# Performance work log

Hardware: AMD Instinct MI355X
Metric: run time of the kernel (lower is better)

## Reference

```python
import jax, jax.numpy as jnp
import numpy as np

B, S = 4096, 8192

def setup_inputs() -> dict:
    key = jax.random.key(0)
    c = jax.random.normal(key, (B, S), dtype=jnp.float32)
    beta = jnp.asarray(10.0, dtype=jnp.float32)
    return {"c": c, "beta": beta}

def reference(c, beta):
    # Original per-step recurrence:
    #   delta_i = (1/beta) * logsumexp([beta*delta_{i-1}, beta*(c_i + delta_{i-1})])
    #           = delta_{i-1} + (1/beta) * log(1 + exp(beta * c_i))
    # i.e. an exact prefix sum of softplus(beta*c)/beta along S.
    # (Note: the torch code stacks delta_prev, not 0, as the first branch,
    #  so the logsumexp telescopes to a cumulative sum.)
    step = jax.nn.softplus(beta * c) / beta          # (B, S)
    return jnp.cumsum(step, axis=1)                  # (B, S) propagated delays
```

## Files before the change

### kernel.cpp

```cpp
#include <hip/hip_runtime.h>
#include <hip/hip_bf16.h>


#define ROW_S   8192
#define BLOCK_T 256
#define NJ      (ROW_S / 4 / BLOCK_T)
#define NWAVE   (BLOCK_T / 64)

__device__ __forceinline__ float softplus_step(float c, float beta, float inv_beta) {
    float tb = beta * c;
    float a  = fabsf(tb);
    float e  = __expf(-a);
    float l  = __logf(1.0f + e);
    return (fmaxf(tb, 0.0f) + l) * inv_beta;
}

__global__ __launch_bounds__(BLOCK_T) void softplus_cumsum_kernel(
    const float* __restrict__ c,
    const float* __restrict__ beta_p,
    float* __restrict__ out)
{
    __shared__ float wave_sums[NJ][NWAVE];

    const int t    = threadIdx.x;
    const int lane = t & 63;
    const int wave = t >> 6;
    const size_t row_base = (size_t)blockIdx.x * ROW_S;

    const float beta     = beta_p[0];
    const float inv_beta = 1.0f / beta;

    const float4* __restrict__ in4  = (const float4*)(c + row_base);
    float4*       __restrict__ out4 = (float4*)(out + row_base);

    float4 v[NJ];
    #pragma unroll
    for (int j = 0; j < NJ; ++j)
        v[j] = in4[j * BLOCK_T + t];

    float4 r[NJ];
    float  s[NJ];
    #pragma unroll
    for (int j = 0; j < NJ; ++j) {
        float a = softplus_step(v[j].x, beta, inv_beta);
        float b = softplus_step(v[j].y, beta, inv_beta);
        float d = softplus_step(v[j].z, beta, inv_beta);
        float e = softplus_step(v[j].w, beta, inv_beta);
        r[j].x = a;
        r[j].y = a + b;
        r[j].z = r[j].y + d;
        r[j].w = r[j].z + e;
        s[j]   = r[j].w;
    }

    float xscan[NJ];
    #pragma unroll
    for (int j = 0; j < NJ; ++j) {
        float x = s[j];
        #pragma unroll
        for (int d = 1; d < 64; d <<= 1) {
            float y = __shfl_up(x, d, 64);
            if (lane >= d) x += y;
        }
        xscan[j] = x;
        if (lane == 63) wave_sums[j][wave] = x;
    }
    __syncthreads();

    float carry = 0.0f;
    #pragma unroll
    for (int j = 0; j < NJ; ++j) {
        float woff = 0.0f, btot = 0.0f;
        #pragma unroll
        for (int w = 0; w < NWAVE; ++w) {
            float ws = wave_sums[j][w];
            if (w < wave) woff += ws;
            btot += ws;
        }
        const float off = carry + woff + (xscan[j] - s[j]);
        carry += btot;

        float4 o;
        o.x = r[j].x + off;
        o.y = r[j].y + off;
        o.z = r[j].z + off;
        o.w = r[j].w + off;
        out4[j * BLOCK_T + t] = o;
    }
}

extern "C" void kernel_launch(void* const* d_in, const int* in_sizes, int n_in,
                              void* d_out, int out_size, void* d_ws, size_t ws_size,
                              hipStream_t stream) {
    const float* c      = (const float*)d_in[0];
    const float* beta_p = (const float*)d_in[1];
    float*       out    = (float*)d_out;

    const int B = in_sizes[0] / ROW_S;
    softplus_cumsum_kernel<<<dim3(B), dim3(BLOCK_T), 0, stream>>>(c, beta_p, out);
}
```

Before: 233.1 us.

## Process four rows per block with register double-buffered prefetch of next row

Each block now handles RPB=4 rows strided by gridDim, issuing the loads for the next row before computing the scan on the current one so memory latency overlaps compute. Wave sums in shared memory are double-buffered by row parity so only one barrier per row is needed. The grid shrinks to B/4 blocks and launch bounds request 4 waves per SIMD, which doubles register use for the input buffers and may cap occupancy or cause spills.

```diff
diff --git a/kernel.cpp b/kernel.cpp
--- a/kernel.cpp
+++ b/kernel.cpp
@@ -6,86 +6,104 @@
 #define BLOCK_T 256
 #define NJ      (ROW_S / 4 / BLOCK_T)
 #define NWAVE   (BLOCK_T / 64)
+#define RPB     4
 
 __device__ __forceinline__ float softplus_step(float c, float beta, float inv_beta) {
     float tb = beta * c;
-    float a  = fabsf(tb);
-    float e  = __expf(-a);
+    float e  = __expf(-fabsf(tb));
     float l  = __logf(1.0f + e);
     return (fmaxf(tb, 0.0f) + l) * inv_beta;
 }
 
-__global__ __launch_bounds__(BLOCK_T) void softplus_cumsum_kernel(
+__global__ __launch_bounds__(BLOCK_T, 4) void softplus_cumsum_kernel(
     const float* __restrict__ c,
     const float* __restrict__ beta_p,
-    float* __restrict__ out)
+    float* __restrict__ out,
+    int nrows)
 {
-    __shared__ float wave_sums[NJ][NWAVE];
+    __shared__ float wave_sums[2][NJ][NWAVE];
 
     const int t    = threadIdx.x;
     const int lane = t & 63;
     const int wave = t >> 6;
-    const size_t row_base = (size_t)blockIdx.x * ROW_S;
 
     const float beta     = beta_p[0];
     const float inv_beta = 1.0f / beta;
 
-    const float4* __restrict__ in4  = (const float4*)(c + row_base);
-    float4*       __restrict__ out4 = (float4*)(out + row_base);
-
-    float4 v[NJ];
-    #pragma unroll
-    for (int j = 0; j < NJ; ++j)
-        v[j] = in4[j * BLOCK_T + t];
-
-    float4 r[NJ];
-    float  s[NJ];
-    #pragma unroll
-    for (int j = 0; j < NJ; ++j) {
-        float a = softplus_step(v[j].x, beta, inv_beta);
-        float b = softplus_step(v[j].y, beta, inv_beta);
-        float d = softplus_step(v[j].z, beta, inv_beta);
-        float e = softplus_step(v[j].w, beta, inv_beta);
-        r[j].x = a;
-        r[j].y = a + b;
-        r[j].z = r[j].y + d;
-        r[j].w = r[j].z + e;
-        s[j]   = r[j].w;
+    float4 va[NJ], vb[NJ];
+    {
+        const size_t row0 = blockIdx.x;
+        if ((int)row0 < nrows) {
+            const float4* in4 = (const float4*)c + row0 * (ROW_S / 4);
+            #pragma unroll
+            for (int j = 0; j < NJ; ++j) va[j] = in4[j * BLOCK_T + t];
+        }
     }
 
-    float xscan[NJ];
     #pragma unroll
-    for (int j = 0; j < NJ; ++j) {
-        float x = s[j];
+    for (int k = 0; k < RPB; ++k) {
+        const size_t row = (size_t)blockIdx.x + (size_t)k * gridDim.x;
+        if ((int)row >= nrows) break;
+
+        const size_t nrow = (size_t)blockIdx.x + (size_t)(k + 1) * gridDim.x;
+        if (k + 1 < RPB && (int)nrow < nrows) {
+            const float4* nin4 = (const float4*)c + nrow * (ROW_S / 4);
+            #pragma unroll
+            for (int j = 0; j < NJ; ++j) vb[j] = nin4[j * BLOCK_T + t];
+        }
+
+        float4 r[NJ];
+        float  s[NJ];
         #pragma unroll
-        for (int d = 1; d < 64; d <<= 1) {
-            float y = __shfl_up(x, d, 64);
-            if (lane >= d) x += y;
+        for (int j = 0; j < NJ; ++j) {
+            float a = softplus_step(va[j].x, beta, inv_beta);
+            float b = softplus_step(va[j].y, beta, inv_beta);
+            float d = softplus_step(va[j].z, beta, inv_beta);
+            float e = softplus_step(va[j].w, beta, inv_beta);
+            r[j].x = a;
+            r[j].y = a + b;
+            r[j].z = r[j].y + d;
+            r[j].w = r[j].z + e;
+            s[j]   = r[j].w;
         }
-        xscan[j] = x;
-        if (lane == 63) wave_sums[j][wave] = x;
-    }
-    __syncthreads();
 
-    float carry = 0.0f;
-    #pragma unroll
-    for (int j = 0; j < NJ; ++j) {
-        float woff = 0.0f, btot = 0.0f;
+        float excl[NJ];
         #pragma unroll
-        for (int w = 0; w < NWAVE; ++w) {
-            float ws = wave_sums[j][w];
-            if (w < wave) woff += ws;
-            btot += ws;
+        for (int j = 0; j < NJ; ++j) {
+            float x = s[j];
+            #pragma unroll
+            for (int d = 1; d < 64; d <<= 1) {
+                float y = __shfl_up(x, d, 64);
+                if (lane >= d) x += y;
+            }
+            excl[j] = x - s[j];
+            if (lane == 63) wave_sums[k & 1][j][wave] = x;
         }
-        const float off = carry + woff + (xscan[j] - s[j]);
-        carry += btot;
+        __syncthreads();
 
-        float4 o;
-        o.x = r[j].x + off;
-        o.y = r[j].y + off;
-        o.z = r[j].z + off;
-        o.w = r[j].w + off;
-        out4[j * BLOCK_T + t] = o;
+        float4* out4 = (float4*)out + row * (ROW_S / 4);
+        float carry = 0.0f;
+        #pragma unroll
+        for (int j = 0; j < NJ; ++j) {
+            float woff = 0.0f, btot = 0.0f;
+            #pragma unroll
+            for (int w = 0; w < NWAVE; ++w) {
+                float ws = wave_sums[k & 1][j][w];
+                if (w < wave) woff += ws;
+                btot += ws;
+            }
+            const float off = carry + woff + excl[j];
+            carry += btot;
+            float4 o;
+            o.x = r[j].x + off;
+            o.y = r[j].y + off;
+            o.z = r[j].z + off;
+            o.w = r[j].w + off;
+            out4[j * BLOCK_T + t] = o;
+        }
+
+        #pragma unroll
+        for (int j = 0; j < NJ; ++j) va[j] = vb[j];
     }
 }
 
@@ -97,5 +115,7 @@
     float*       out    = (float*)d_out;
 
     const int B = in_sizes[0] / ROW_S;
-    softplus_cumsum_kernel<<<dim3(B), dim3(BLOCK_T), 0, stream>>>(c, beta_p, out);
+    const int nblocks = (B + RPB - 1) / RPB;
+    softplus_cumsum_kernel<<<dim3(nblocks), dim3(BLOCK_T), 0, stream>>>(
+        c, beta_p, out, B);
 }
```

New measurement: 237.9 us. 2.1% more time.

## Assign one wavefront per row with double-buffered chunked loads and no LDS sync

Applied to the files above, without the earlier changes.

Each row is now handled by a single 64-lane wavefront instead of a full 256-thread block. The row is processed in 32 sequential chunks of 256 floats, each scanned with a wave shuffle, and a running carry is kept in a register. This removes the shared-memory wave-sum exchange and the block barrier. Loads for the next group of 8 chunks are issued while the current group is computed (a two-buffer register pipeline), and the launch bounds request higher occupancy. In exchange, each wave runs a long serial chain of scans per row, and a row is read in 1 KB strides per chunk rather than all at once.

```diff
diff --git a/kernel.cpp b/kernel.cpp
--- a/kernel.cpp
+++ b/kernel.cpp
@@ -4,88 +4,77 @@
 
 #define ROW_S   8192
 #define BLOCK_T 256
-#define NJ      (ROW_S / 4 / BLOCK_T)
-#define NWAVE   (BLOCK_T / 64)
+#define CHUNK   64
+#define NCH     8
+#define NG      4
 
 __device__ __forceinline__ float softplus_step(float c, float beta, float inv_beta) {
     float tb = beta * c;
-    float a  = fabsf(tb);
-    float e  = __expf(-a);
+    float e  = __expf(-fabsf(tb));
     float l  = __logf(1.0f + e);
     return (fmaxf(tb, 0.0f) + l) * inv_beta;
 }
 
-__global__ __launch_bounds__(BLOCK_T) void softplus_cumsum_kernel(
+__global__ __launch_bounds__(BLOCK_T, 4) void softplus_cumsum_kernel(
     const float* __restrict__ c,
     const float* __restrict__ beta_p,
     float* __restrict__ out)
 {
-    __shared__ float wave_sums[NJ][NWAVE];
-
-    const int t    = threadIdx.x;
-    const int lane = t & 63;
-    const int wave = t >> 6;
-    const size_t row_base = (size_t)blockIdx.x * ROW_S;
+    const int lane = threadIdx.x & 63;
+    const int row  = blockIdx.x * (BLOCK_T / 64) + (threadIdx.x >> 6);
 
     const float beta     = beta_p[0];
     const float inv_beta = 1.0f / beta;
 
-    const float4* __restrict__ in4  = (const float4*)(c + row_base);
-    float4*       __restrict__ out4 = (float4*)(out + row_base);
+    const float4* __restrict__ in4  = (const float4*)c   + (size_t)row * (ROW_S / 4);
+    float4*       __restrict__ out4 = (float4*)out       + (size_t)row * (ROW_S / 4);
 
-    float4 v[NJ];
+    float4 v[2][NCH];
+
     #pragma unroll
-    for (int j = 0; j < NJ; ++j)
-        v[j] = in4[j * BLOCK_T + t];
-
-    float4 r[NJ];
-    float  s[NJ];
-    #pragma unroll
-    for (int j = 0; j < NJ; ++j) {
-        float a = softplus_step(v[j].x, beta, inv_beta);
-        float b = softplus_step(v[j].y, beta, inv_beta);
-        float d = softplus_step(v[j].z, beta, inv_beta);
-        float e = softplus_step(v[j].w, beta, inv_beta);
-        r[j].x = a;
-        r[j].y = a + b;
-        r[j].z = r[j].y + d;
-        r[j].w = r[j].z + e;
-        s[j]   = r[j].w;
-    }
-
-    float xscan[NJ];
-    #pragma unroll
-    for (int j = 0; j < NJ; ++j) {
-        float x = s[j];
-        #pragma unroll
-        for (int d = 1; d < 64; d <<= 1) {
-            float y = __shfl_up(x, d, 64);
-            if (lane >= d) x += y;
-        }
-        xscan[j] = x;
-        if (lane == 63) wave_sums[j][wave] = x;
-    }
-    __syncthreads();
+    for (int ch = 0; ch < NCH; ++ch)
+        v[0][ch] = in4[ch * CHUNK + lane];
 
     float carry = 0.0f;
+
     #pragma unroll
-    for (int j = 0; j < NJ; ++j) {
-        float woff = 0.0f, btot = 0.0f;
+    for (int g = 0; g < NG; ++g) {
+        const int cur = g & 1;
+        const int nxt = cur ^ 1;
+
+        if (g + 1 < NG) {
+            #pragma unroll
+            for (int ch = 0; ch < NCH; ++ch)
+                v[nxt][ch] = in4[(g + 1) * NCH * CHUNK + ch * CHUNK + lane];
+        }
+
         #pragma unroll
-        for (int w = 0; w < NWAVE; ++w) {
-            float ws = wave_sums[j][w];
-            if (w < wave) woff += ws;
-            btot += ws;
+        for (int ch = 0; ch < NCH; ++ch) {
+            float4 e = v[cur][ch];
+            float p0 = softplus_step(e.x, beta, inv_beta);
+            float p1 = p0 + softplus_step(e.y, beta, inv_beta);
+            float p2 = p1 + softplus_step(e.z, beta, inv_beta);
+            float p3 = p2 + softplus_step(e.w, beta, inv_beta);
+
+            float x = p3;
+            #pragma unroll
+            for (int d = 1; d < 64; d <<= 1) {
+                float y = __shfl_up(x, d, 64);
+                if (lane >= d) x += y;
+            }
+            const float excl = x - p3;
+            const float tot  = __shfl(x, 63, 64);
+
+            const float off = carry + excl;
+            float4 o;
+            o.x = off + p0;
+            o.y = off + p1;
+            o.z = off + p2;
+            o.w = off + p3;
+            out4[g * NCH * CHUNK + ch * CHUNK + lane] = o;
+
+            carry += tot;
         }
-        const float off = carry + woff + (xscan[j] - s[j]);
-        carry += btot;
-
-        float4 o;
-        o.x = r[j].x + off;
-        o.y = r[j].y + off;
-        o.z = r[j].z + off;
-        o.w = r[j].w + off;
-        out4[j * BLOCK_T + t] = o;
     }
 }
 
@@ -97,5 +86,8 @@
     float*       out    = (float*)d_out;
 
     const int B = in_sizes[0] / ROW_S;
-    softplus_cumsum_kernel<<<dim3(B), dim3(BLOCK_T), 0, stream>>>(c, beta_p, out);
+    const int waves_per_block = BLOCK_T / 64;
+    const int nblocks = B / waves_per_block;
+    softplus_cumsum_kernel<<<dim3(nblocks), dim3(BLOCK_T), 0, stream>>>(
+        c, beta_p, out);
 }
```

After: 239.5 us. 2.8% more time.
